# Kernel optimization log

Hardware: AMD Instinct MI355X
Metric: run time of the kernel (lower is better)

## Reference

```python
import jax, jax.numpy as jnp
import numpy as np

B, N, K = 8, 2048, 16
C_IN, C_MID, C_OUT = 64, 16, 64
WH = [32, 32]
FH = [256]


def _mlp_params(key, dims, scale_keyed=True):
    ps = []
    for i in range(len(dims) - 1):
        key, k1 = jax.random.split(key)
        w = jax.random.normal(k1, (dims[i], dims[i + 1]), jnp.float32) / np.sqrt(dims[i])
        b = jnp.zeros((dims[i + 1],), jnp.float32)
        ps += [w, b]
    return ps


def setup_inputs() -> dict:
    key = jax.random.key(0)
    k1, k2, k3, k4, k5 = jax.random.split(key, 5)
    groups = jnp.broadcast_to(jnp.arange(N, dtype=jnp.int32) // K, (B, N))
    points = jax.random.normal(k1, (B, N, 3), jnp.float32)
    feats = jax.random.normal(k2, (B, N, C_IN), jnp.float32)
    point_mask = (jax.random.uniform(k3, (B, N)) > 0.1).astype(jnp.float32)
    w1, b1, w2, b2, w3, b3 = _mlp_params(k4, [3] + WH + [C_MID])
    f1, fb1, f2, fb2 = _mlp_params(k5, [C_IN * C_MID] + FH + [C_OUT])
    return {"groups": groups, "points": points, "feats": feats,
            "point_mask": point_mask,
            "w1": w1, "b1": b1, "w2": w2, "b2": b2, "w3": w3, "b3": b3,
            "f1": f1, "fb1": fb1, "f2": f2, "fb2": fb2}


def _neighbor_idxs(groups):
    # matches[b,i,j] = groups[b,i]==groups[b,j]; torch .nonzero yields, per (b,i),
    # the matching j in increasing order -> stable argsort of ~matches, take first K.
    matches = groups[:, :, None] == groups[:, None, :]            # [B,N,N]
    return jnp.argsort((~matches).astype(jnp.int32), axis=-1)[:, :, :K]  # [B,N,K]


def reference(groups, points, feats, point_mask,
              w1, b1, w2, b2, w3, b3, f1, fb1, f2, fb2):
    idxs = _neighbor_idxs(groups)                                  # [B,N,K] int
    gather = jax.vmap(lambda arr, ix: arr[ix])                     # per-batch gather
    nb_pts = gather(points, idxs)                                  # [B,N,K,3]
    nb_feats = gather(feats, idxs)                                 # [B,N,K,C_IN]
    rel = points[:, :, None, :] - nb_pts                           # [B,N,K,3] (xy encoding = identity)

    # weight_conv: pointwise MLP 3 -> 32 -> 32 -> C_MID, then explicit ReLU
    h = jax.nn.relu(rel @ w1 + b1)
    h = jax.nn.relu(h @ w2 + b2)
    m = jax.nn.relu(h @ w3 + b3)                                   # [B,N,K,C_MID]

    tmask = gather(point_mask, idxs)                               # [B,N,K]
    m = m * tmask[..., None]
    nb_feats = nb_feats * tmask[..., None]

    # per-(point) matmul: [C_MID,K] x [K,C_IN] -> flatten C_MID-major
    e = jnp.einsum('bnkm,bnkc->bnmc', m, nb_feats)                 # [B,N,C_MID,C_IN]
    e = e.reshape(B, N, C_MID * C_IN)

    # final_conv: pointwise MLP 1024 -> 256 -> C_OUT
    h2 = jax.nn.relu(e @ f1 + fb1)
    out = h2 @ f2 + fb2                                            # [B,N,C_OUT]
    return out
```

## Files before the change

### kernel.cpp

```cpp
#include <hip/hip_runtime.h>

typedef unsigned short u16;
typedef short bf16x8 __attribute__((ext_vector_type(8)));
typedef float f32x4  __attribute__((ext_vector_type(4)));
typedef u16   u16x4  __attribute__((ext_vector_type(4)));

__device__ __forceinline__ u16 f2bf(float f) {
  union { float f; unsigned int i; } v; v.f = f;
  unsigned int r = (v.i + 0x7FFFu + ((v.i >> 16) & 1u)) >> 16;
  return (u16)r;
}

__global__ __launch_bounds__(256) void repack_k(const float* __restrict__ f1,
                                                const float* __restrict__ f2,
                                                u16* __restrict__ f1p,
                                                u16* __restrict__ f2p) {
  const int o = blockIdx.x * 256 + threadIdx.x;
  if (o < 262144) {
    const int j = o & 7, n = (o >> 3) & 255, kb = o >> 11;
    f1p[o] = f2bf(f1[(kb * 8 + j) * 256 + n]);
  }
  if (o < 16384) {
    const int j = o & 7, n = (o >> 3) & 63, kb = o >> 9;
    f2p[o] = f2bf(f2[(kb * 8 + j) * 64 + n]);
  }
}

__global__ __launch_bounds__(256, 4) void mlp_einsum_k(
    const float* __restrict__ points, const float* __restrict__ feats,
    const float* __restrict__ pmask,
    const float* __restrict__ w1, const float* __restrict__ b1,
    const float* __restrict__ w2, const float* __restrict__ b2,
    const float* __restrict__ w3, const float* __restrict__ b3,
    const float* __restrict__ f1, const float* __restrict__ f2,
    u16* __restrict__ f1p, u16* __restrict__ f2p,
    u16* __restrict__ Eg) {
  const int gi = blockIdx.x;
  const int bb = blockIdx.y;
  const int base = gi * 16;
  const int t = threadIdx.x;

  __shared__ float Pl[16][3];
  __shared__ float Mask[16];
  __shared__ float F[1024];
  __shared__ float Ml[16 * 260];

  {
    const int o = (bb * 128 + gi) * 256 + t;
    { const int j = o & 7, n = (o >> 3) & 255, kb = o >> 11;
      f1p[o] = f2bf(f1[(kb * 8 + j) * 256 + n]); }
    if (o < 16384) {
      const int j = o & 7, n = (o >> 3) & 63, kb = o >> 9;
      f2p[o] = f2bf(f2[(kb * 8 + j) * 64 + n]);
    }
  }

  if (t < 16) {
    Mask[t] = pmask[bb * 2048 + base + t];
    const int p = (bb * 2048 + base + t) * 3;
    Pl[t][0] = points[p + 0];
    Pl[t][1] = points[p + 1];
    Pl[t][2] = points[p + 2];
  }
  __syncthreads();

  {
    const int k = t >> 4;
    const float mk = Mask[k];
    const f32x4 fv =
        *(const f32x4*)&feats[(size_t)(bb * 2048 + base) * 64 + t * 4];
    f32x4 fs = { fv.x * mk, fv.y * mk, fv.z * mk, fv.w * mk };
    *(f32x4*)&F[t * 4] = fs;
  }
  {
    const int i = t >> 4, k = t & 15;
    const float r0 = Pl[i][0] - Pl[k][0];
    const float r1 = Pl[i][1] - Pl[k][1];
    const float r2 = Pl[i][2] - Pl[k][2];
    float h1[32];
#pragma unroll
    for (int o = 0; o < 32; ++o) {
      float a = b1[o];
      a = fmaf(r0, w1[o], a);
      a = fmaf(r1, w1[32 + o], a);
      a = fmaf(r2, w1[64 + o], a);
      h1[o] = fmaxf(a, 0.f);
    }
    float h2[32];
#pragma unroll
    for (int o = 0; o < 32; ++o) h2[o] = b2[o];
#pragma unroll
    for (int j = 0; j < 32; ++j) {
      const float hj = h1[j];
      const float* w = &w2[j * 32];
#pragma unroll
      for (int o = 0; o < 32; ++o) h2[o] = fmaf(hj, w[o], h2[o]);
    }
#pragma unroll
    for (int o = 0; o < 32; ++o) h2[o] = fmaxf(h2[o], 0.f);
    float mo[16];
#pragma unroll
    for (int o = 0; o < 16; ++o) mo[o] = b3[o];
#pragma unroll
    for (int j = 0; j < 32; ++j) {
      const float hj = h2[j];
      const float* w = &w3[j * 16];
#pragma unroll
      for (int o = 0; o < 16; ++o) mo[o] = fmaf(hj, w[o], mo[o]);
    }
    const float mk = Mask[k];
    float* Mrow = &Ml[i * 260 + k * 16];
#pragma unroll
    for (int o = 0; o < 16; ++o) Mrow[o] = fmaxf(mo[o], 0.f) * mk;
  }
  __syncthreads();

  {
    const int i = t >> 4;
    const int c0 = (t & 15) * 4;
    u16* Erow = Eg + (size_t)(bb * 2048 + base + i) * 1024;
#pragma unroll
    for (int half = 0; half < 2; ++half) {
      float acc[8][4] = {};
#pragma unroll
      for (int k = 0; k < 16; ++k) {
        const float* Fr = &F[k * 64 + c0];
        const float f0 = Fr[0], fA = Fr[1], fB = Fr[2], fC = Fr[3];
        const float* Mv = &Ml[i * 260 + k * 16 + half * 8];
#pragma unroll
        for (int mi = 0; mi < 8; ++mi) {
          const float mv = Mv[mi];
          acc[mi][0] = fmaf(mv, f0, acc[mi][0]);
          acc[mi][1] = fmaf(mv, fA, acc[mi][1]);
          acc[mi][2] = fmaf(mv, fB, acc[mi][2]);
          acc[mi][3] = fmaf(mv, fC, acc[mi][3]);
        }
      }
#pragma unroll
      for (int mi = 0; mi < 8; ++mi) {
        u16x4 v = { f2bf(acc[mi][0]), f2bf(acc[mi][1]),
                    f2bf(acc[mi][2]), f2bf(acc[mi][3]) };
        *(u16x4*)&Erow[(half * 8 + mi) * 64 + c0] = v;
      }
    }
  }
}

#define STAGE(bf_, kc_)                                                        \
  do {                                                                         \
    const int rl_ = lane >> 3;              \
    const int sg_ = (lane & 7) ^ rl_;         \
    const u16* s0_ =                                                           \
        Eg + (size_t)(R + wv * 8 + rl_) * 1024 + (kc_) + sg_ * 8;              \
    u16* d0_ = &Asw[bf_][(wv * 8) * 64];            \
    __builtin_amdgcn_global_load_lds(                                          \
        (const __attribute__((address_space(1))) void*)s0_,                    \
        (__attribute__((address_space(3))) void*)d0_, 16, 0, 0);               \
  } while (0)

__global__ __launch_bounds__(512) void gemm_k(
    const u16* __restrict__ Eg, const u16* __restrict__ f1p,
    const float* __restrict__ fb1, const u16* __restrict__ f2p,
    const float* __restrict__ fb2, float* __restrict__ out) {
  const int R = blockIdx.x * 64;
  const int t = threadIdx.x;
  const int wv = t >> 6, lane = t & 63;
  const int wr = wv >> 2, wc = wv & 3;
  const int q = lane >> 4, r16 = lane & 15;

  __shared__ __align__(16) u16 Asw[3][64 * 64];
  __shared__ __align__(16) u16 H2[64 * 264];

  const int nb = wc * 64;
  f32x4 acc[2][4] = {};

  STAGE(0, 0);
  STAGE(1, 64);
  int cur = 0, stg = 2;
  for (int c = 0; c < 16; ++c) {
    if (c < 15) asm volatile("s_waitcnt vmcnt(1)" ::: "memory");
    else        asm volatile("s_waitcnt vmcnt(0)" ::: "memory");
    __builtin_amdgcn_s_barrier();

    bf16x8 bv[2][4];
#pragma unroll
    for (int ksl = 0; ksl < 2; ++ksl) {
      const int kb = c * 8 + ksl * 4 + q;
#pragma unroll
      for (int nt = 0; nt < 4; ++nt)
        bv[ksl][nt] =
            *(const bf16x8*)&f1p[(size_t)(kb * 256 + nb + nt * 16 + r16) * 8];
    }
    bf16x8 a[2][2];
#pragma unroll
    for (int ksl = 0; ksl < 2; ++ksl)
#pragma unroll
      for (int rt = 0; rt < 2; ++rt) {
        const int row = wr * 32 + rt * 16 + r16;
        const int g = (ksl * 4 + q) ^ (row & 7);
        a[ksl][rt] = *(const bf16x8*)&Asw[cur][row * 64 + g * 8];
      }
    __builtin_amdgcn_sched_barrier(0);
    if (c <= 13) STAGE(stg, (c + 2) * 64);
    __builtin_amdgcn_sched_barrier(0);
#pragma unroll
    for (int ksl = 0; ksl < 2; ++ksl)
#pragma unroll
      for (int nt = 0; nt < 4; ++nt)
#pragma unroll
        for (int rt = 0; rt < 2; ++rt)
          acc[rt][nt] = __builtin_amdgcn_mfma_f32_16x16x32_bf16(
              a[ksl][rt], bv[ksl][nt], acc[rt][nt], 0, 0, 0);
    cur = (cur == 2) ? 0 : cur + 1;
    stg = (stg == 2) ? 0 : stg + 1;
  }

#pragma unroll
  for (int nt = 0; nt < 4; ++nt) {
    const int col = nb + nt * 16 + r16;
    const float bias = fb1[col];
#pragma unroll
    for (int rt = 0; rt < 2; ++rt)
#pragma unroll
      for (int r = 0; r < 4; ++r)
        H2[(wr * 32 + rt * 16 + q * 4 + r) * 264 + col] =
            f2bf(fmaxf(acc[rt][nt][r] + bias, 0.f));
  }
  __syncthreads();

  const int n0 = wc * 16;
  const float bias2 = fb2[n0 + r16];
#pragma unroll
  for (int rt = 0; rt < 2; ++rt) {
    const int rowb = wr * 32 + rt * 16;
    f32x4 a2 = {};
#pragma unroll
    for (int ks = 0; ks < 8; ++ks) {
      const bf16x8 av =
          *(const bf16x8*)&H2[(rowb + r16) * 264 + ks * 32 + q * 8];
      const bf16x8 b2v =
          *(const bf16x8*)&f2p[(size_t)((ks * 4 + q) * 64 + n0 + r16) * 8];
      a2 = __builtin_amdgcn_mfma_f32_16x16x32_bf16(av, b2v, a2, 0, 0, 0);
    }
#pragma unroll
    for (int r = 0; r < 4; ++r)
      out[(size_t)(R + rowb + q * 4 + r) * 64 + n0 + r16] = a2[r] + bias2;
  }
}
#undef STAGE

__global__ __launch_bounds__(256) void fused_k(
    const float* __restrict__ points, const float* __restrict__ feats,
    const float* __restrict__ pmask,
    const float* __restrict__ w1, const float* __restrict__ b1,
    const float* __restrict__ w2, const float* __restrict__ b2,
    const float* __restrict__ w3, const float* __restrict__ b3,
    const u16* __restrict__ f1p, const float* __restrict__ fb1,
    const u16* __restrict__ f2p, const float* __restrict__ fb2,
    float* __restrict__ out) {
  const int gi = blockIdx.x;
  const int bb = blockIdx.y;
  const int base = gi * 16;
  const int t = threadIdx.x;

  __shared__ float Wl[1712];
  __shared__ float Pl[16][3];
  __shared__ float Mask[16];
  __shared__ float F[1024];
  __shared__ __align__(16) u16 E[16 * 1032];
  __shared__ __align__(16) union {
    float Ml[16 * 16 * 17];
    u16   H2[16 * 264];
  } U;

  for (int idx = t; idx < 96;   idx += 256) Wl[idx]        = w1[idx];
  for (int idx = t; idx < 32;   idx += 256) Wl[96 + idx]   = b1[idx];
  for (int idx = t; idx < 1024; idx += 256) Wl[128 + idx]  = w2[idx];
  for (int idx = t; idx < 32;   idx += 256) Wl[1152 + idx] = b2[idx];
  for (int idx = t; idx < 512;  idx += 256) Wl[1184 + idx] = w3[idx];
  for (int idx = t; idx < 16;   idx += 256) Wl[1696 + idx] = b3[idx];
  if (t < 16) {
    Mask[t] = pmask[bb * 2048 + base + t];
    const int p = (bb * 2048 + base + t) * 3;
    Pl[t][0] = points[p + 0];
    Pl[t][1] = points[p + 1];
    Pl[t][2] = points[p + 2];
  }
  __syncthreads();

  for (int e = t; e < 1024; e += 256) {
    const int k = e >> 6;
    F[e] = feats[(bb * 2048 + base) * 64 + e] * Mask[k];
  }
  {
    const int i = t >> 4, k = t & 15;
    const float r0 = Pl[i][0] - Pl[k][0];
    const float r1 = Pl[i][1] - Pl[k][1];
    const float r2 = Pl[i][2] - Pl[k][2];
    float h1[32];
#pragma unroll
    for (int o = 0; o < 32; ++o) {
      float a = Wl[96 + o];
      a = fmaf(r0, Wl[o], a);
      a = fmaf(r1, Wl[32 + o], a);
      a = fmaf(r2, Wl[64 + o], a);
      h1[o] = fmaxf(a, 0.f);
    }
    float h2[32];
#pragma unroll
    for (int o = 0; o < 32; ++o) h2[o] = Wl[1152 + o];
#pragma unroll
    for (int j = 0; j < 32; ++j) {
      const float hj = h1[j];
      const float* w = &Wl[128 + j * 32];
#pragma unroll
      for (int o = 0; o < 32; ++o) h2[o] = fmaf(hj, w[o], h2[o]);
    }
#pragma unroll
    for (int o = 0; o < 32; ++o) h2[o] = fmaxf(h2[o], 0.f);
    float mo[16];
#pragma unroll
    for (int o = 0; o < 16; ++o) mo[o] = Wl[1696 + o];
#pragma unroll
    for (int j = 0; j < 32; ++j) {
      const float hj = h2[j];
      const float* w = &Wl[1184 + j * 16];
#pragma unroll
      for (int o = 0; o < 16; ++o) mo[o] = fmaf(hj, w[o], mo[o]);
    }
    const float mk = Mask[k];
    float* Mrow = &U.Ml[(i * 16 + k) * 17];
#pragma unroll
    for (int o = 0; o < 16; ++o) Mrow[o] = fmaxf(mo[o], 0.f) * mk;
  }
  __syncthreads();

  {
    const int i = t >> 4;
    const int c0 = (t & 15) * 4;
    float acc[16][4] = {};
#pragma unroll
    for (int k = 0; k < 16; ++k) {
      const float* Fr = &F[k * 64 + c0];
      const float f0 = Fr[0], fA = Fr[1], fB = Fr[2], fC = Fr[3];
      const float* Mrow = &U.Ml[(i * 16 + k) * 17];
#pragma unroll
      for (int mi = 0; mi < 16; ++mi) {
        const float mv = Mrow[mi];
        acc[mi][0] = fmaf(mv, f0, acc[mi][0]);
        acc[mi][1] = fmaf(mv, fA, acc[mi][1]);
        acc[mi][2] = fmaf(mv, fB, acc[mi][2]);
        acc[mi][3] = fmaf(mv, fC, acc[mi][3]);
      }
    }
    __syncthreads();
#pragma unroll
    for (int mi = 0; mi < 16; ++mi) {
      u16x4 v = { f2bf(acc[mi][0]), f2bf(acc[mi][1]), f2bf(acc[mi][2]), f2bf(acc[mi][3]) };
      *(u16x4*)&E[i * 1032 + mi * 64 + c0] = v;
    }
  }
  __syncthreads();

  {
    const int wv = t >> 6;
    const int lane = t & 63;
    const int q = lane >> 4, r16 = lane & 15;
    const int nb = wv * 64;
    f32x4 acc[4] = {};
    for (int ks = 0; ks < 32; ++ks) {
      const int k0 = ks * 32;
      const bf16x8 a = *(const bf16x8*)&E[r16 * 1032 + k0 + q * 8];
      const int kb = (k0 >> 3) + q;
#pragma unroll
      for (int nt = 0; nt < 4; ++nt) {
        const bf16x8 bvv = *(const bf16x8*)&f1p[(kb * 256 + nb + nt * 16 + r16) * 8];
        acc[nt] = __builtin_amdgcn_mfma_f32_16x16x32_bf16(a, bvv, acc[nt], 0, 0, 0);
      }
    }
    __syncthreads();
#pragma unroll
    for (int nt = 0; nt < 4; ++nt) {
      const int col = nb + nt * 16 + r16;
      const float bias = fb1[col];
#pragma unroll
      for (int r = 0; r < 4; ++r)
        U.H2[(q * 4 + r) * 264 + col] = f2bf(fmaxf(acc[nt][r] + bias, 0.f));
    }
  }
  __syncthreads();

  {
    const int wv = t >> 6;
    const int lane = t & 63;
    const int q = lane >> 4, r16 = lane & 15;
    const int n0 = wv * 16;
    f32x4 acc = {};
#pragma unroll
    for (int ks = 0; ks < 8; ++ks) {
      const int k0 = ks * 32;
      const bf16x8 a = *(const bf16x8*)&U.H2[r16 * 264 + k0 + q * 8];
      const bf16x8 bvv = *(const bf16x8*)&f2p[(((k0 >> 3) + q) * 64 + n0 + r16) * 8];
      acc = __builtin_amdgcn_mfma_f32_16x16x32_bf16(a, bvv, acc, 0, 0, 0);
    }
    const int col = n0 + r16;
    const float bias = fb2[col];
#pragma unroll
    for (int r = 0; r < 4; ++r) {
      const int row = q * 4 + r;
      out[((size_t)(bb * 2048 + base + row)) * 64 + col] = acc[r] + bias;
    }
  }
}

extern "C" void kernel_launch(void* const* d_in, const int* in_sizes, int n_in,
                              void* d_out, int out_size, void* d_ws, size_t ws_size,
                              hipStream_t stream) {
  const float* points = (const float*)d_in[1];
  const float* feats  = (const float*)d_in[2];
  const float* pmask  = (const float*)d_in[3];
  const float* w1 = (const float*)d_in[4];
  const float* b1 = (const float*)d_in[5];
  const float* w2 = (const float*)d_in[6];
  const float* b2 = (const float*)d_in[7];
  const float* w3 = (const float*)d_in[8];
  const float* b3 = (const float*)d_in[9];
  const float* f1 = (const float*)d_in[10];
  const float* fb1 = (const float*)d_in[11];
  const float* f2 = (const float*)d_in[12];
  const float* fb2 = (const float*)d_in[13];
  float* out = (float*)d_out;

  u16* f1p = (u16*)d_ws;
  u16* f2p = f1p + 262144;
  const size_t NEED = 524288 + 32768 + (size_t)16384 * 1024 * 2;

  if (ws_size >= NEED) {
    u16* Eg = f2p + 16384;
    mlp_einsum_k<<<dim3(128, 8), dim3(256), 0, stream>>>(
        points, feats, pmask, w1, b1, w2, b2, w3, b3, f1, f2, f1p, f2p, Eg);
    gemm_k<<<dim3(256), dim3(512), 0, stream>>>(Eg, f1p, fb1, f2p, fb2, out);
  } else {
    repack_k<<<dim3(1024), dim3(256), 0, stream>>>(f1, f2, f1p, f2p);
    fused_k<<<dim3(128, 8), dim3(256), 0, stream>>>(points, feats, pmask,
                                                    w1, b1, w2, b2, w3, b3,
                                                    f1p, fb1, f2p, fb2, out);
  }
}
```

Baseline: 132.6 us.

## Prefetch f1 weight fragments one chunk ahead in the gemm k-loop

```diff
diff --git a/kernel.cpp b/kernel.cpp
--- a/kernel.cpp
+++ b/kernel.cpp
@@ -55,6 +55,9 @@
     }
   }
 
+  const f32x4 fv =
+      *(const f32x4*)&feats[(size_t)(bb * 2048 + base) * 64 + t * 4];
+
   if (t < 16) {
     Mask[t] = pmask[bb * 2048 + base + t];
     const int p = (bb * 2048 + base + t) * 3;
@@ -67,8 +70,6 @@
   {
     const int k = t >> 4;
     const float mk = Mask[k];
-    const f32x4 fv =
-        *(const f32x4*)&feats[(size_t)(bb * 2048 + base) * 64 + t * 4];
     f32x4 fs = { fv.x * mk, fv.y * mk, fv.z * mk, fv.w * mk };
     *(f32x4*)&F[t * 4] = fs;
   }
@@ -146,7 +147,7 @@
   }
 }
 
-#define STAGE(bf_, kc_)                                                        \
+#define STAGE_A(bf_, kc_)                                                      \
   do {                                                                         \
     const int rl_ = lane >> 3;              \
     const int sg_ = (lane & 7) ^ rl_;         \
@@ -158,6 +159,42 @@
         (__attribute__((address_space(3))) void*)d0_, 16, 0, 0);               \
   } while (0)
 
+#define LOAD_B(c_, bv_)                                                        \
+  do {                                                                         \
+    _Pragma("unroll")                                                          \
+    for (int ksl = 0; ksl < 2; ++ksl) {                                        \
+      const int kb = (c_) * 8 + ksl * 4 + q;                                   \
+      _Pragma("unroll")                                                        \
+      for (int nt = 0; nt < 4; ++nt)                                           \
+        bv_[ksl][nt] = *(const bf16x8*)                                        \
+            &f1p[(size_t)(kb * 256 + nb + nt * 16 + r16) * 8];                 \
+    }                                                                          \
+  } while (0)
+
+#define READ_A(ring_, a_)                                                      \
+  do {                                                                         \
+    _Pragma("unroll")                                                          \
+    for (int ksl = 0; ksl < 2; ++ksl)                                          \
+      _Pragma("unroll")                                                        \
+      for (int rt = 0; rt < 2; ++rt) {                                         \
+        const int row = wr * 32 + rt * 16 + r16;                               \
+        const int g = (ksl * 4 + q) ^ (row & 7);                               \
+        a_[ksl][rt] = *(const bf16x8*)&Asw[ring_][row * 64 + g * 8];           \
+      }                                                                        \
+  } while (0)
+
+#define MFMA8(a_, bv_)                                                         \
+  do {                                                                         \
+    _Pragma("unroll")                                                          \
+    for (int ksl = 0; ksl < 2; ++ksl)                                          \
+      _Pragma("unroll")                                                        \
+      for (int nt = 0; nt < 4; ++nt)                                           \
+        _Pragma("unroll")                                                      \
+        for (int rt = 0; rt < 2; ++rt)                                         \
+          acc[rt][nt] = __builtin_amdgcn_mfma_f32_16x16x32_bf16(               \
+              a_[ksl][rt], bv_[ksl][nt], acc[rt][nt], 0, 0, 0);                \
+  } while (0)
+
 __global__ __launch_bounds__(512) void gemm_k(
     const u16* __restrict__ Eg, const u16* __restrict__ f1p,
     const float* __restrict__ fb1, const u16* __restrict__ f2p,
@@ -174,45 +211,31 @@
   const int nb = wc * 64;
   f32x4 acc[2][4] = {};
 
-  STAGE(0, 0);
-  STAGE(1, 64);
-  int cur = 0, stg = 2;
-  for (int c = 0; c < 16; ++c) {
-    if (c < 15) asm volatile("s_waitcnt vmcnt(1)" ::: "memory");
-    else        asm volatile("s_waitcnt vmcnt(0)" ::: "memory");
+  STAGE_A(0, 0);
+  STAGE_A(1, 64);
+  bf16x8 bvA[2][4], bvB[2][4];
+  LOAD_B(0, bvA);
+
+  for (int cc = 0; cc < 16; cc += 2) {
+    asm volatile("s_waitcnt vmcnt(9)" ::: "memory");
     __builtin_amdgcn_s_barrier();
-
-    bf16x8 bv[2][4];
-#pragma unroll
-    for (int ksl = 0; ksl < 2; ++ksl) {
-      const int kb = c * 8 + ksl * 4 + q;
-#pragma unroll
-      for (int nt = 0; nt < 4; ++nt)
-        bv[ksl][nt] =
-            *(const bf16x8*)&f1p[(size_t)(kb * 256 + nb + nt * 16 + r16) * 8];
-    }
-    bf16x8 a[2][2];
-#pragma unroll
-    for (int ksl = 0; ksl < 2; ++ksl)
-#pragma unroll
-      for (int rt = 0; rt < 2; ++rt) {
-        const int row = wr * 32 + rt * 16 + r16;
-        const int g = (ksl * 4 + q) ^ (row & 7);
-        a[ksl][rt] = *(const bf16x8*)&Asw[cur][row * 64 + g * 8];
-      }
     __builtin_amdgcn_sched_barrier(0);
-    if (c <= 13) STAGE(stg, (c + 2) * 64);
+    bf16x8 aA[2][2];
+    READ_A(cc % 3, aA);
+    LOAD_B(cc + 1, bvB);
+    if (cc <= 13) STAGE_A((cc + 2) % 3, (cc + 2) * 64);
     __builtin_amdgcn_sched_barrier(0);
-#pragma unroll
-    for (int ksl = 0; ksl < 2; ++ksl)
-#pragma unroll
-      for (int nt = 0; nt < 4; ++nt)
-#pragma unroll
-        for (int rt = 0; rt < 2; ++rt)
-          acc[rt][nt] = __builtin_amdgcn_mfma_f32_16x16x32_bf16(
-              a[ksl][rt], bv[ksl][nt], acc[rt][nt], 0, 0, 0);
-    cur = (cur == 2) ? 0 : cur + 1;
-    stg = (stg == 2) ? 0 : stg + 1;
+    MFMA8(aA, bvA);
+    if (cc < 14) asm volatile("s_waitcnt vmcnt(9)" ::: "memory");
+    else         asm volatile("s_waitcnt vmcnt(8)" ::: "memory");
+    __builtin_amdgcn_s_barrier();
+    __builtin_amdgcn_sched_barrier(0);
+    bf16x8 aB[2][2];
+    READ_A((cc + 1) % 3, aB);
+    if (cc < 14) LOAD_B(cc + 2, bvA);
+    if (cc <= 12) STAGE_A((cc + 3) % 3, (cc + 3) * 64);
+    __builtin_amdgcn_sched_barrier(0);
+    MFMA8(aB, bvB);
   }
 
 #pragma unroll
@@ -247,7 +270,10 @@
       out[(size_t)(R + rowb + q * 4 + r) * 64 + n0 + r16] = a2[r] + bias2;
   }
 }
-#undef STAGE
+#undef STAGE_A
+#undef LOAD_B
+#undef READ_A
+#undef MFMA8
 
 __global__ __launch_bounds__(256) void fused_k(
     const float* __restrict__ points, const float* __restrict__ feats,
```

Result: no change. 132.7 us (+0.1%).
